# Kernel tuning notes

Hardware: AMD Instinct MI355X
Metric: run time of the kernel (lower is better)

The kernel has to match this reference:

```python
import jax, jax.numpy as jnp
import numpy as np

N, E = 50000, 800000
IN_C, H_C, OUT_C, HEADS = 64, 32, 32, 8


def setup_inputs() -> dict:
    key = jax.random.key(0)
    ks = jax.random.split(key, 16)
    def glorot(k, shape):
        fan_in = shape[-1]
        return jax.random.normal(k, shape, dtype=jnp.float32) / jnp.sqrt(jnp.float32(fan_in))
    inp = {
        'x': jax.random.normal(ks[0], (N, IN_C), dtype=jnp.float32),
        'edge_index': jax.random.randint(ks[1], (2, E), 0, N, dtype=jnp.int64),
        # layer 1: in_c -> h_c, heads
        'W1l': glorot(ks[2], (HEADS * H_C, IN_C)),
        'b1l': jnp.zeros((HEADS * H_C,), jnp.float32),
        'W1r': glorot(ks[3], (HEADS * H_C, IN_C)),
        'b1r': jnp.zeros((HEADS * H_C,), jnp.float32),
        'att1': glorot(ks[4], (HEADS, H_C)),
        'bias1': jnp.zeros((H_C,), jnp.float32),
        # layer 2: h_c -> out_c, heads
        'W2l': glorot(ks[5], (HEADS * OUT_C, H_C)),
        'b2l': jnp.zeros((HEADS * OUT_C,), jnp.float32),
        'W2r': glorot(ks[6], (HEADS * OUT_C, H_C)),
        'b2r': jnp.zeros((HEADS * OUT_C,), jnp.float32),
        'att2': glorot(ks[7], (HEADS, OUT_C)),
        'bias2': jnp.zeros((OUT_C,), jnp.float32),
    }
    return inp


def _gatv2_layer(x, src, dst, valid, Wl, bl, Wr, br, att, bias):
    # PyG GATv2Conv (share_weights=False, concat=False): message j->i uses
    # e = att . leaky_relu(lin_l(x_j) + lin_r(x_i), 0.2); softmax over dst; agg lin_l(x_j).
    n = x.shape[0]
    heads, c = att.shape
    xl = (x @ Wl.T + bl).reshape(n, heads, c)
    xr = (x @ Wr.T + br).reshape(n, heads, c)
    m = jax.nn.leaky_relu(xl[src] + xr[dst], negative_slope=0.2)  # [Etot,H,C]
    score = jnp.einsum('ehc,hc->eh', m, att)                      # [Etot,H]
    score = jnp.where(valid[:, None], score, -jnp.inf)
    smax = jax.ops.segment_max(score, dst, num_segments=n)        # [N,H]
    a = jnp.where(valid[:, None], jnp.exp(score - smax[dst]), 0.0)
    denom = jax.ops.segment_sum(a, dst, num_segments=n)
    a = a / jnp.maximum(denom[dst], 1e-16)
    out = jax.ops.segment_sum(a[..., None] * xl[src], dst, num_segments=n)  # [N,H,C]
    return out.mean(axis=1) + bias


def reference(x, edge_index, W1l, b1l, W1r, b1r, att1, bias1,
              W2l, b2l, W2r, b2r, att2, bias2):
    n = x.shape[0]
    src0, dst0 = edge_index[0], edge_index[1]
    # PyG removes existing self loops then adds fresh ones: mask originals,
    # append one self loop per node (keeps static shapes).
    loop = jnp.arange(n, dtype=src0.dtype)
    src = jnp.concatenate([src0, loop])
    dst = jnp.concatenate([dst0, loop])
    valid = jnp.concatenate([src0 != dst0, jnp.ones((n,), bool)])
    h = _gatv2_layer(x, src, dst, valid, W1l, b1l, W1r, b1r, att1, bias1)
    h = jax.nn.leaky_relu(h, negative_slope=0.01)  # nn.LeakyReLU default
    out = _gatv2_layer(h, src, dst, valid, W2l, b2l, W2r, b2r, att2, bias2)
    return out
```

## Files before the change

kernel.cpp:

```cpp
#include <hip/hip_runtime.h>
#include <math.h>

#define HEADS 8
#define CDIM 32
#define ODIM 256
#define BKT_SHIFT 7
#define CHUNK 2048

typedef _Float16 h2 __attribute__((ext_vector_type(2)));
typedef _Float16 h4 __attribute__((ext_vector_type(4)));
typedef _Float16 h8 __attribute__((ext_vector_type(8)));
typedef float f32x4 __attribute__((ext_vector_type(4)));
union H4 { h4 v; h2 p[2]; };

#if __has_builtin(__builtin_amdgcn_fdot2)
#define FDOT2(a,b,c) __builtin_amdgcn_fdot2((a),(b),(c),false)
#else
static __device__ __forceinline__ float fdot2_sw(h2 a, h2 b, float c){
  return fmaf((float)a.x, (float)b.x, fmaf((float)a.y, (float)b.y, c));
}
#define FDOT2(a,b,c) fdot2_sw((a),(b),(c))
#endif

__device__ __forceinline__ float lrelu(float v, float s){ return fmaxf(v, s*v); }


__global__ __launch_bounds__(512) void csr_offs_kernel(
    int* __restrict__ hist, int* __restrict__ btotal, int NB, int B){
  __shared__ int s[512];
  int b = blockIdx.x, t = threadIdx.x;
  int v = (t < NB) ? hist[t*B + b] : 0;
  s[t] = v;
  __syncthreads();
  for (int off=1; off<512; off<<=1){
    int u = (t >= off) ? s[t-off] : 0;
    __syncthreads(); s[t] += u; __syncthreads();
  }
  int excl = s[t] - v;
  if (t < NB) hist[t*B + b] = excl;
  if (t == NB-1) btotal[b] = excl + v;
}

__global__ __launch_bounds__(512) void csr_base_kernel(
    const int* __restrict__ btotal, int* __restrict__ base, int B){
  __shared__ int s[512];
  int t = threadIdx.x;
  int v = (t < B) ? btotal[t] : 0;
  s[t] = v;
  __syncthreads();
  for (int off=1; off<512; off<<=1){
    int u = (t >= off) ? s[t-off] : 0;
    __syncthreads(); s[t] += u; __syncthreads();
  }
  if (t < B) base[t] = s[t] - v;
  if (t == B-1) base[B] = s[t];
}

__global__ __launch_bounds__(256) void csr_scatter_kernel(
    const int* __restrict__ src, const int* __restrict__ dst,
    const int* __restrict__ rank, const int* __restrict__ offs,
    const int* __restrict__ base, int* __restrict__ bpack, int e, int B){
  int t = threadIdx.x, k = blockIdx.x;
  int base_i = k*CHUNK;
#pragma unroll
  for (int j = 0; j < CHUNK/256; ++j){
    int i = base_i + j*256 + t;
    if (i < e){
      int r = rank[i];
      if (r >= 0){
        int d = dst[i], s = src[i];
        int b = d >> BKT_SHIFT;
        int pos = base[b] + offs[k*B + b] + r;
        bpack[pos] = (s << BKT_SHIFT) | (d & 127);
      }
    }
  }
}

__global__ __launch_bounds__(256) void csr_sort_kernel(
    const int* __restrict__ bpack, const int* __restrict__ base,
    int* __restrict__ csr, int* __restrict__ indptr, int n, int B){
  __shared__ int lh[128], cur[128], ss[128];
  int b = blockIdx.x, t = threadIdx.x;
  int beg = base[b], cnt = base[b+1] - beg;
  if (t < 128) lh[t] = 0;
  __syncthreads();
  for (int j = t; j < cnt; j += 256){
    int p = bpack[beg + j];
    atomicAdd(&lh[p & 127], 1);
  }
  __syncthreads();
  int v = (t < 128) ? lh[t] : 0;
  if (t < 128) ss[t] = v;
  __syncthreads();
  for (int off=1; off<128; off<<=1){
    int u = (t >= off && t < 128) ? ss[t-off] : 0;
    __syncthreads();
    if (t < 128) ss[t] += u;
    __syncthreads();
  }
  if (t < 128){
    int excl = ss[t] - v;
    cur[t] = excl;
    int node = (b << BKT_SHIFT) + t;
    if (node <= n) indptr[node] = beg + excl;
  }
  __syncthreads();
  for (int j = t; j < cnt; j += 256){
    int p = bpack[beg + j];
    int lpos = atomicAdd(&cur[p & 127], 1);
    csr[beg + lpos] = p >> BKT_SHIFT;
  }
}

template<int K, bool FUSE_HIST>
__global__ __launch_bounds__(256, 2) void gemm_mfma(const float* __restrict__ X,
    const float* __restrict__ Wl, const float* __restrict__ bl,
    const float* __restrict__ Wr, const float* __restrict__ br,
    _Float16* __restrict__ outl, _Float16* __restrict__ outr, int n,
    const int* __restrict__ src, const int* __restrict__ dst,
    int* __restrict__ rank, int* __restrict__ hist, int e, int B){
  if (FUSE_HIST && blockIdx.y == 2){
    int k = blockIdx.x;
    int NB = (e + CHUNK-1)/CHUNK;
    if (k >= NB) return;
    __shared__ int lh[512];
    int t = threadIdx.x;
    for (int b = t; b < B; b += 256) lh[b] = 0;
    __syncthreads();
    int base_i = k*CHUNK;
#pragma unroll
    for (int j = 0; j < CHUNK/256; ++j){
      int i = base_i + j*256 + t;
      if (i < e){
        int s = src[i], d = dst[i];
        int r = -1;
        if (s != d) r = atomicAdd(&lh[d>>BKT_SHIFT], 1);
        rank[i] = r;
      }
    }
    __syncthreads();
    for (int b = t; b < B; b += 256) hist[k*B + b] = lh[b];
    return;
  }
  const int KP = K + 8;
  __shared__ __align__(16) _Float16 Xs[64*(K+8)];
  int t = threadIdx.x;
  int n0 = blockIdx.x*64;
  int ybase = blockIdx.y;

  for (int idx = t; idx < 64*(K/4); idx += 256){
    int row = idx/(K/4), c = (idx%(K/4))*4;
    int node = n0 + row; if (node >= n) node = n-1;
    float4 xv = *(const float4*)(X + (size_t)node*K + c);
    h4 hv = {(_Float16)xv.x, (_Float16)xv.y, (_Float16)xv.z, (_Float16)xv.w};
    *(h4*)(Xs + row*KP + c) = hv;
  }
  __syncthreads();

  int wave = t >> 6, lane = t & 63;
  int co = ybase*256 + wave*64;
  const float* W   = (co < 256) ? Wl : Wr;
  const float* Bv  = (co < 256) ? bl : br;
  _Float16* outp   = (co < 256) ? outl : outr;
  int lco = co & 255;
  int lr = lane & 15, lg = lane >> 4;

  f32x4 acc[4][4];
#pragma unroll
  for (int c = 0; c < 4; ++c)
#pragma unroll
    for (int m = 0; m < 4; ++m) acc[c][m] = (f32x4){0.f, 0.f, 0.f, 0.f};

#pragma unroll
  for (int ks = 0; ks < K/32; ++ks){
    int k0 = ks*32 + lg*8;
    h8 a[4], b[4];
#pragma unroll
    for (int c = 0; c < 4; ++c){
      const float* wp = W + (size_t)(lco + c*16 + lr)*K + k0;
      float4 w0 = *(const float4*)(wp);
      float4 w1 = *(const float4*)(wp + 4);
      a[c] = (h8){(_Float16)w0.x,(_Float16)w0.y,(_Float16)w0.z,(_Float16)w0.w,
                  (_Float16)w1.x,(_Float16)w1.y,(_Float16)w1.z,(_Float16)w1.w};
    }
#pragma unroll
    for (int m = 0; m < 4; ++m)
      b[m] = *(const h8*)(Xs + (m*16 + lr)*KP + k0);
#pragma unroll
    for (int c = 0; c < 4; ++c)
#pragma unroll
      for (int m = 0; m < 4; ++m)
        acc[c][m] = __builtin_amdgcn_mfma_f32_16x16x32_f16(a[c], b[m], acc[c][m], 0, 0, 0);
  }

#pragma unroll
  for (int c = 0; c < 4; ++c){
    int ch = lco + c*16 + lg*4;
    float4 bb = *(const float4*)(Bv + ch);
#pragma unroll
    for (int m = 0; m < 4; ++m){
      int node = n0 + m*16 + lr;
      if (node < n){
        h4 o = {(_Float16)(acc[c][m][0] + bb.x), (_Float16)(acc[c][m][1] + bb.y),
                (_Float16)(acc[c][m][2] + bb.z), (_Float16)(acc[c][m][3] + bb.w)};
        *(h4*)(outp + (size_t)node*ODIM + ch) = o;
      }
    }
  }
}

__global__ __launch_bounds__(256) void edge_kernel(
    const _Float16* __restrict__ xl, const _Float16* __restrict__ xr,
    const float* __restrict__ att, const float* __restrict__ bias,
    const int* __restrict__ indptr, const int* __restrict__ csr_src,
    float* __restrict__ out, int n, int act)
{
  int wid = blockIdx.x*4 + (threadIdx.x >> 6);
  if (wid >= n) return;
  int lane = threadIdx.x & 63;
  const float LOG2E = 1.44269504088896341f;

  float4 attf = *(const float4*)(att + 4*lane);
  h2 at0 = (h2){(_Float16)(attf.x*LOG2E), (_Float16)(attf.y*LOG2E)};
  h2 at1 = (h2){(_Float16)(attf.z*LOG2E), (_Float16)(attf.w*LOG2E)};
  const h2 c02 = {(_Float16)0.2f, (_Float16)0.2f};

  H4 xrh; xrh.v = *(const h4*)(xr + (size_t)wid*ODIM + 4*lane);
  H4 self; self.v = *(const h4*)(xl + (size_t)wid*ODIM + 4*lane);

  auto score = [&](const H4& c)->float{
    h2 t0 = c.p[0] + xrh.p[0];
    h2 t1 = c.p[1] + xrh.p[1];
    h2 q0 = __builtin_elementwise_max(t0, t0 * c02);
    h2 q1 = __builtin_elementwise_max(t1, t1 * c02);
    float d = FDOT2(q0, at0, FDOT2(q1, at1, 0.f));
    d += __shfl_xor(d, 1);
    d += __shfl_xor(d, 2);
    d += __shfl_xor(d, 4);
    return d;
  };

  float w0 = exp2f(score(self));
  float denom = w0;
  float4 acc;
  acc.x = w0 * (float)self.v.x;
  acc.y = w0 * (float)self.v.y;
  acc.z = w0 * (float)self.v.z;
  acc.w = w0 * (float)self.v.w;

  int beg = __builtin_amdgcn_readfirstlane(indptr[wid]);
  int end = __builtin_amdgcn_readfirstlane(indptr[wid+1]);
  int cnt = end - beg;

#define GATHER(j) (*(const h4*)(xl + (size_t)((unsigned)__shfl(sidx,(j)))*ODIM + 4*lane))
  for (int cb = 0; cb < cnt; cb += 64){
    int ccnt = min(cnt - cb, 64);
    int sidx = (lane < ccnt) ? csr_src[beg + cb + lane] : 0;
    H4 r0, r1, r2, r3;
    r0.v = (h4){}; r1.v = (h4){}; r2.v = (h4){}; r3.v = (h4){};
    if (ccnt > 0) r0.v = GATHER(0);
    if (ccnt > 1) r1.v = GATHER(1);
    if (ccnt > 2) r2.v = GATHER(2);
    if (ccnt > 3) r3.v = GATHER(3);
#pragma unroll 2
    for (int k = 0; k < ccnt; k += 2){
      H4 e0 = r0, e1 = r1;
      r0 = r2; r1 = r3;
      if (k+4 < ccnt) r2.v = GATHER(k+4);
      if (k+5 < ccnt) r3.v = GATHER(k+5);
      float s0 = score(e0);
      float s1 = score(e1);
      float pe0 = exp2f(s0);
      float pe1 = (k+1 < ccnt) ? exp2f(s1) : 0.f;
      denom += pe0 + pe1;
      acc.x = fmaf(pe0, (float)e0.v.x, fmaf(pe1, (float)e1.v.x, acc.x));
      acc.y = fmaf(pe0, (float)e0.v.y, fmaf(pe1, (float)e1.v.y, acc.y));
      acc.z = fmaf(pe0, (float)e0.v.z, fmaf(pe1, (float)e1.v.z, acc.z));
      acc.w = fmaf(pe0, (float)e0.v.w, fmaf(pe1, (float)e1.v.w, acc.w));
    }
  }
#undef GATHER

  float inv = 1.f/denom;
  float vx = acc.x*inv, vy = acc.y*inv, vz = acc.z*inv, vw = acc.w*inv;
  vx += __shfl_xor(vx, 8);  vx += __shfl_xor(vx, 16);  vx += __shfl_xor(vx, 32);
  vy += __shfl_xor(vy, 8);  vy += __shfl_xor(vy, 16);  vy += __shfl_xor(vy, 32);
  vz += __shfl_xor(vz, 8);  vz += __shfl_xor(vz, 16);  vz += __shfl_xor(vz, 32);
  vw += __shfl_xor(vw, 8);  vw += __shfl_xor(vw, 16);  vw += __shfl_xor(vw, 32);
  if (lane < 8){
    float4 bv = *(const float4*)(bias + 4*lane);
    float ox = vx*0.125f + bv.x;
    float oy = vy*0.125f + bv.y;
    float oz = vz*0.125f + bv.z;
    float ow = vw*0.125f + bv.w;
    if (act){
      ox = lrelu(ox, 0.01f); oy = lrelu(oy, 0.01f);
      oz = lrelu(oz, 0.01f); ow = lrelu(ow, 0.01f);
    }
    *(float4*)(out + (size_t)wid*CDIM + 4*lane) = make_float4(ox, oy, oz, ow);
  }
}

extern "C" void kernel_launch(void* const* d_in, const int* in_sizes, int n_in,
                              void* d_out, int out_size, void* d_ws, size_t ws_size,
                              hipStream_t stream){
  (void)n_in; (void)out_size; (void)ws_size;
  const float* x    = (const float*)d_in[0];
  const int*   ei   = (const int*)d_in[1];
  const float* W1l  = (const float*)d_in[2];
  const float* b1l  = (const float*)d_in[3];
  const float* W1r  = (const float*)d_in[4];
  const float* b1r  = (const float*)d_in[5];
  const float* att1 = (const float*)d_in[6];
  const float* bias1= (const float*)d_in[7];
  const float* W2l  = (const float*)d_in[8];
  const float* b2l  = (const float*)d_in[9];
  const float* W2r  = (const float*)d_in[10];
  const float* b2r  = (const float*)d_in[11];
  const float* att2 = (const float*)d_in[12];
  const float* bias2= (const float*)d_in[13];
  int n = in_sizes[0] / 64;
  int e = in_sizes[1] / 2;
  const int* src = ei;
  const int* dst = ei + e;

  char* ws = (char*)d_ws;
  size_t off = 0;
  auto alloc = [&](size_t bytes)->char*{
    char* p = ws + off; off += (bytes + 255) & ~(size_t)255; return p;
  };
  _Float16* xl  = (_Float16*)alloc((size_t)n*ODIM*2);
  _Float16* xr  = (_Float16*)alloc((size_t)n*ODIM*2);
  float* h      = (float*)alloc((size_t)n*CDIM*4);
  int*   indptr = (int*)alloc((size_t)(n+1)*4);
  int*   rank   = (int*)alloc((size_t)e*4);
  int*   csr    = (int*)alloc((size_t)e*4);
  int*   bpack  = (int*)alloc((size_t)e*4);

  int NB = (e + CHUNK-1) / CHUNK;
  int B  = (n + 127) >> 7;
  int*   hist   = (int*)alloc((size_t)NB*B*4);
  int*   btotal = (int*)alloc((size_t)B*4);
  int*   base   = (int*)alloc((size_t)(B+1)*4);

  int nt64 = (n + 63) / 64;

  gemm_mfma<64,true><<<dim3(nt64,3), 256, 0, stream>>>(
      x, W1l, b1l, W1r, b1r, xl, xr, n, src, dst, rank, hist, e, B);
  csr_offs_kernel<<<B, 512, 0, stream>>>(hist, btotal, NB, B);
  csr_base_kernel<<<1, 512, 0, stream>>>(btotal, base, B);
  csr_scatter_kernel<<<NB, 256, 0, stream>>>(src, dst, rank, hist, base, bpack, e, B);
  csr_sort_kernel<<<B, 256, 0, stream>>>(bpack, base, csr, indptr, n, B);

  edge_kernel<<<(n+3)/4, 256, 0, stream>>>(xl, xr, att1, bias1, indptr, csr, h, n, 1);
  gemm_mfma<32,false><<<dim3(nt64,2), 256, 0, stream>>>(
      h, W2l, b2l, W2r, b2r, xl, xr, n, nullptr, nullptr, nullptr, nullptr, 0, 0);
  edge_kernel<<<(n+3)/4, 256, 0, stream>>>(xl, xr, att2, bias2, indptr, csr, (float*)d_out, n, 0);
}
```

Before: 310.5 us.

## Split edge aggregation per head and process eight edges per wavefront concurrently

The per-node edge kernel now launches one wavefront per node and head. Each group of 8 lanes handles a different neighbor edge, so eight edges are gathered in parallel instead of a serial prefetch chain over all heads. Per-head partial results go to a new fp32 buffer, and a separate reduction kernel averages heads, adds bias and applies the activation. This trades extra launches, repeated CSR index reads per head and an n×256 fp32 intermediate write/read for more memory-level parallelism in the gather.

Result: slower. 526.2 us (+69.4%).

```diff
diff --git a/kernel.cpp b/kernel.cpp
--- a/kernel.cpp
+++ b/kernel.cpp
@@ -210,28 +210,30 @@
   }
 }
 
-__global__ __launch_bounds__(256) void edge_kernel(
+__global__ __launch_bounds__(256) void edge_head_kernel(
     const _Float16* __restrict__ xl, const _Float16* __restrict__ xr,
-    const float* __restrict__ att, const float* __restrict__ bias,
+    const float* __restrict__ att,
     const int* __restrict__ indptr, const int* __restrict__ csr_src,
-    float* __restrict__ out, int n, int act)
+    float* __restrict__ part, int n)
 {
-  int wid = blockIdx.x*4 + (threadIdx.x >> 6);
-  if (wid >= n) return;
+  int head = blockIdx.x & 7;
+  int node = ((blockIdx.x >> 3) << 2) + (threadIdx.x >> 6);
+  if (node >= n) return;
   int lane = threadIdx.x & 63;
+  int g = lane >> 3, q = lane & 7;
   const float LOG2E = 1.44269504088896341f;
 
-  float4 attf = *(const float4*)(att + 4*lane);
+  float4 attf = *(const float4*)(att + head*32 + 4*q);
   h2 at0 = (h2){(_Float16)(attf.x*LOG2E), (_Float16)(attf.y*LOG2E)};
   h2 at1 = (h2){(_Float16)(attf.z*LOG2E), (_Float16)(attf.w*LOG2E)};
   const h2 c02 = {(_Float16)0.2f, (_Float16)0.2f};
 
-  H4 xrh; xrh.v = *(const h4*)(xr + (size_t)wid*ODIM + 4*lane);
-  H4 self; self.v = *(const h4*)(xl + (size_t)wid*ODIM + 4*lane);
-
-  auto score = [&](const H4& c)->float{
-    h2 t0 = c.p[0] + xrh.p[0];
-    h2 t1 = c.p[1] + xrh.p[1];
+  const _Float16* xlh = xl + head*32 + 4*q;
+  H4 xr4; xr4.v = *(const h4*)(xr + (size_t)node*ODIM + head*32 + 4*q);
+
+  auto scoreh = [&](const H4& c)->float{
+    h2 t0 = c.p[0] + xr4.p[0];
+    h2 t1 = c.p[1] + xr4.p[1];
     h2 q0 = __builtin_elementwise_max(t0, t0 * c02);
     h2 q1 = __builtin_elementwise_max(t1, t1 * c02);
     float d = FDOT2(q0, at0, FDOT2(q1, at1, 0.f));
@@ -241,65 +243,64 @@
     return d;
   };
 
-  float w0 = exp2f(score(self));
-  float denom = w0;
+  H4 self; self.v = *(const h4*)(xlh + (size_t)node*ODIM);
+  float w0 = exp2f(scoreh(self));
+  float gz = (g == 0) ? w0 : 0.f;
+  float denom = gz;
   float4 acc;
-  acc.x = w0 * (float)self.v.x;
-  acc.y = w0 * (float)self.v.y;
-  acc.z = w0 * (float)self.v.z;
-  acc.w = w0 * (float)self.v.w;
-
-  int beg = __builtin_amdgcn_readfirstlane(indptr[wid]);
-  int end = __builtin_amdgcn_readfirstlane(indptr[wid+1]);
+  acc.x = gz * (float)self.v.x;
+  acc.y = gz * (float)self.v.y;
+  acc.z = gz * (float)self.v.z;
+  acc.w = gz * (float)self.v.w;
+
+  int beg = __builtin_amdgcn_readfirstlane(indptr[node]);
+  int end = __builtin_amdgcn_readfirstlane(indptr[node+1]);
   int cnt = end - beg;
 
-#define GATHER(j) (*(const h4*)(xl + (size_t)((unsigned)__shfl(sidx,(j)))*ODIM + 4*lane))
   for (int cb = 0; cb < cnt; cb += 64){
     int ccnt = min(cnt - cb, 64);
-    int sidx = (lane < ccnt) ? csr_src[beg + cb + lane] : 0;
-    H4 r0, r1, r2, r3;
-    r0.v = (h4){}; r1.v = (h4){}; r2.v = (h4){}; r3.v = (h4){};
-    if (ccnt > 0) r0.v = GATHER(0);
-    if (ccnt > 1) r1.v = GATHER(1);
-    if (ccnt > 2) r2.v = GATHER(2);
-    if (ccnt > 3) r3.v = GATHER(3);
+    int sidx = (lane < ccnt) ? csr_src[beg + cb + lane] : node;
 #pragma unroll 2
-    for (int k = 0; k < ccnt; k += 2){
-      H4 e0 = r0, e1 = r1;
-      r0 = r2; r1 = r3;
-      if (k+4 < ccnt) r2.v = GATHER(k+4);
-      if (k+5 < ccnt) r3.v = GATHER(k+5);
-      float s0 = score(e0);
-      float s1 = score(e1);
-      float pe0 = exp2f(s0);
-      float pe1 = (k+1 < ccnt) ? exp2f(s1) : 0.f;
-      denom += pe0 + pe1;
-      acc.x = fmaf(pe0, (float)e0.v.x, fmaf(pe1, (float)e1.v.x, acc.x));
-      acc.y = fmaf(pe0, (float)e0.v.y, fmaf(pe1, (float)e1.v.y, acc.y));
-      acc.z = fmaf(pe0, (float)e0.v.z, fmaf(pe1, (float)e1.v.z, acc.z));
-      acc.w = fmaf(pe0, (float)e0.v.w, fmaf(pe1, (float)e1.v.w, acc.w));
-    }
-  }
-#undef GATHER
-
-  float inv = 1.f/denom;
-  float vx = acc.x*inv, vy = acc.y*inv, vz = acc.z*inv, vw = acc.w*inv;
-  vx += __shfl_xor(vx, 8);  vx += __shfl_xor(vx, 16);  vx += __shfl_xor(vx, 32);
-  vy += __shfl_xor(vy, 8);  vy += __shfl_xor(vy, 16);  vy += __shfl_xor(vy, 32);
-  vz += __shfl_xor(vz, 8);  vz += __shfl_xor(vz, 16);  vz += __shfl_xor(vz, 32);
-  vw += __shfl_xor(vw, 8);  vw += __shfl_xor(vw, 16);  vw += __shfl_xor(vw, 32);
-  if (lane < 8){
-    float4 bv = *(const float4*)(bias + 4*lane);
-    float ox = vx*0.125f + bv.x;
-    float oy = vy*0.125f + bv.y;
-    float oz = vz*0.125f + bv.z;
-    float ow = vw*0.125f + bv.w;
-    if (act){
-      ox = lrelu(ox, 0.01f); oy = lrelu(oy, 0.01f);
-      oz = lrelu(oz, 0.01f); ow = lrelu(ow, 0.01f);
-    }
-    *(float4*)(out + (size_t)wid*CDIM + 4*lane) = make_float4(ox, oy, oz, ow);
-  }
+    for (int k = 0; k < ccnt; k += 8){
+      int j = k + g;
+      int si = __shfl(sidx, j);
+      H4 cv; cv.v = *(const h4*)(xlh + (size_t)si*ODIM);
+      float sc = scoreh(cv);
+      float pe = (j < ccnt) ? exp2f(sc) : 0.f;
+      denom += pe;
+      acc.x = fmaf(pe, (float)cv.v.x, acc.x);
+      acc.y = fmaf(pe, (float)cv.v.y, acc.y);
+      acc.z = fmaf(pe, (float)cv.v.z, acc.z);
+      acc.w = fmaf(pe, (float)cv.v.w, acc.w);
+    }
+  }
+
+#pragma unroll
+  for (int off = 8; off < 64; off <<= 1){
+    denom += __shfl_xor(denom, off);
+    acc.x += __shfl_xor(acc.x, off);
+    acc.y += __shfl_xor(acc.y, off);
+    acc.z += __shfl_xor(acc.z, off);
+    acc.w += __shfl_xor(acc.w, off);
+  }
+  if (g == 0){
+    float inv = 1.f/denom;
+    float* pp = part + ((size_t)node*HEADS + head)*CDIM + 4*q;
+    pp[0] = acc.x*inv; pp[1] = acc.y*inv; pp[2] = acc.z*inv; pp[3] = acc.w*inv;
+  }
+}
+
+__global__ __launch_bounds__(256) void head_reduce_kernel(
+    const float* __restrict__ part, const float* __restrict__ bias,
+    float* __restrict__ out, int n, int act){
+  int idx = blockIdx.x*256 + threadIdx.x;
+  int node = idx >> 5, c = idx & 31;
+  if (node >= n) return;
+  const float* p = part + (size_t)node*(HEADS*CDIM) + c;
+  float s = p[0]+p[32]+p[64]+p[96]+p[128]+p[160]+p[192]+p[224];
+  float o = s*0.125f + bias[c];
+  if (act) o = lrelu(o, 0.01f);
+  out[(size_t)node*CDIM + c] = o;
 }
 
 extern "C" void kernel_launch(void* const* d_in, const int* in_sizes, int n_in,
@@ -333,6 +334,7 @@
   _Float16* xl  = (_Float16*)alloc((size_t)n*ODIM*2);
   _Float16* xr  = (_Float16*)alloc((size_t)n*ODIM*2);
   float* h      = (float*)alloc((size_t)n*CDIM*4);
+  float* part   = (float*)alloc((size_t)n*HEADS*CDIM*4);
   int*   indptr = (int*)alloc((size_t)(n+1)*4);
   int*   rank   = (int*)alloc((size_t)e*4);
   int*   csr    = (int*)alloc((size_t)e*4);
@@ -345,6 +347,8 @@
   int*   base   = (int*)alloc((size_t)(B+1)*4);
 
   int nt64 = (n + 63) / 64;
+  int nq   = (n + 3) / 4;
+  int nrc  = (n*CDIM + 255) / 256;
 
   gemm_mfma<64,true><<<dim3(nt64,3), 256, 0, stream>>>(
       x, W1l, b1l, W1r, b1r, xl, xr, n, src, dst, rank, hist, e, B);
@@ -353,8 +357,10 @@
   csr_scatter_kernel<<<NB, 256, 0, stream>>>(src, dst, rank, hist, base, bpack, e, B);
   csr_sort_kernel<<<B, 256, 0, stream>>>(bpack, base, csr, indptr, n, B);
 
-  edge_kernel<<<(n+3)/4, 256, 0, stream>>>(xl, xr, att1, bias1, indptr, csr, h, n, 1);
+  edge_head_kernel<<<nq*8, 256, 0, stream>>>(xl, xr, att1, indptr, csr, part, n);
+  head_reduce_kernel<<<nrc, 256, 0, stream>>>(part, bias1, h, n, 1);
   gemm_mfma<32,false><<<dim3(nt64,2), 256, 0, stream>>>(
       h, W2l, b2l, W2r, b2r, xl, xr, n, nullptr, nullptr, nullptr, nullptr, 0, 0);
-  edge_kernel<<<(n+3)/4, 256, 0, stream>>>(xl, xr, att2, bias2, indptr, csr, (float*)d_out, n, 0);
-}
+  edge_head_kernel<<<nq*8, 256, 0, stream>>>(xl, xr, att2, indptr, csr, part, n);
+  head_reduce_kernel<<<nrc, 256, 0, stream>>>(part, bias2, (float*)d_out, n, 0);
+}
```

## Pre-convert weights to fp16, widen GEMM blocks to 512 threads, add nontemporal hints

Applied to the files above, without the earlier changes.

A small kernel now converts all four weight matrices to fp16 once per call. The GEMM then loads h8 fragments directly instead of converting fp32 to fp16 in every wave. Each GEMM block grows to 512 threads and covers both the left and right projections for a 64-node tile, so the X tile is staged and converted once instead of twice. The histogram side-blocks are adapted to the new block size. Nontemporal loads and stores are added for the X tile, the xr row, the CSR indices and the edge output, which adds one extra launch and lowers per-SM occupancy flexibility.

Measured after the change: 302.7 us. 2.5% less time.

```diff
diff --git a/kernel.cpp b/kernel.cpp
--- a/kernel.cpp
+++ b/kernel.cpp
@@ -11,7 +11,8 @@
 typedef _Float16 h4 __attribute__((ext_vector_type(4)));
 typedef _Float16 h8 __attribute__((ext_vector_type(8)));
 typedef float f32x4 __attribute__((ext_vector_type(4)));
-union H4 { h4 v; h2 p[2]; };
+typedef unsigned long long u64;
+union H4 { h4 v; h2 p[2]; u64 u; };
 
 #if __has_builtin(__builtin_amdgcn_fdot2)
 #define FDOT2(a,b,c) __builtin_amdgcn_fdot2((a),(b),(c),false)
@@ -23,6 +24,21 @@
 #endif
 
 __device__ __forceinline__ float lrelu(float v, float s){ return fmaxf(v, s*v); }
+
+__global__ __launch_bounds__(256) void wcvt_kernel(
+    const float* __restrict__ W1l, const float* __restrict__ W1r,
+    const float* __restrict__ W2l, const float* __restrict__ W2r,
+    _Float16* __restrict__ w1lh, _Float16* __restrict__ w1rh,
+    _Float16* __restrict__ w2lh, _Float16* __restrict__ w2rh){
+  int i = (blockIdx.x*256 + threadIdx.x)*4;
+  const float* s; _Float16* d; int off;
+  if (i < 16384)      { s = W1l; d = w1lh; off = i; }
+  else if (i < 32768) { s = W1r; d = w1rh; off = i - 16384; }
+  else if (i < 40960) { s = W2l; d = w2lh; off = i - 32768; }
+  else                { s = W2r; d = w2rh; off = i - 40960; }
+  float4 v = *(const float4*)(s + off);
+  *(h4*)(d + off) = (h4){(_Float16)v.x, (_Float16)v.y, (_Float16)v.z, (_Float16)v.w};
+}
 
 
 __global__ __launch_bounds__(512) void csr_offs_kernel(
@@ -114,24 +130,24 @@
 }
 
 template<int K, bool FUSE_HIST>
-__global__ __launch_bounds__(256, 2) void gemm_mfma(const float* __restrict__ X,
-    const float* __restrict__ Wl, const float* __restrict__ bl,
-    const float* __restrict__ Wr, const float* __restrict__ br,
+__global__ __launch_bounds__(512) void gemm_mfma(const float* __restrict__ X,
+    const _Float16* __restrict__ Wlh, const float* __restrict__ bl,
+    const _Float16* __restrict__ Wrh, const float* __restrict__ br,
     _Float16* __restrict__ outl, _Float16* __restrict__ outr, int n,
     const int* __restrict__ src, const int* __restrict__ dst,
     int* __restrict__ rank, int* __restrict__ hist, int e, int B){
-  if (FUSE_HIST && blockIdx.y == 2){
+  if (FUSE_HIST && blockIdx.y == 1){
     int k = blockIdx.x;
     int NB = (e + CHUNK-1)/CHUNK;
     if (k >= NB) return;
     __shared__ int lh[512];
     int t = threadIdx.x;
-    for (int b = t; b < B; b += 256) lh[b] = 0;
+    if (t < 512) lh[t] = 0;
     __syncthreads();
     int base_i = k*CHUNK;
 #pragma unroll
-    for (int j = 0; j < CHUNK/256; ++j){
-      int i = base_i + j*256 + t;
+    for (int j = 0; j < CHUNK/512; ++j){
+      int i = base_i + j*512 + t;
       if (i < e){
         int s = src[i], d = dst[i];
         int r = -1;
@@ -140,29 +156,28 @@
       }
     }
     __syncthreads();
-    for (int b = t; b < B; b += 256) hist[k*B + b] = lh[b];
+    for (int b = t; b < B; b += 512) hist[k*B + b] = lh[b];
     return;
   }
   const int KP = K + 8;
   __shared__ __align__(16) _Float16 Xs[64*(K+8)];
   int t = threadIdx.x;
   int n0 = blockIdx.x*64;
-  int ybase = blockIdx.y;
-
-  for (int idx = t; idx < 64*(K/4); idx += 256){
+
+  for (int idx = t; idx < 64*(K/4); idx += 512){
     int row = idx/(K/4), c = (idx%(K/4))*4;
     int node = n0 + row; if (node >= n) node = n-1;
-    float4 xv = *(const float4*)(X + (size_t)node*K + c);
-    h4 hv = {(_Float16)xv.x, (_Float16)xv.y, (_Float16)xv.z, (_Float16)xv.w};
-    *(h4*)(Xs + row*KP + c) = hv;
+    f32x4 xv = __builtin_nontemporal_load((const f32x4*)(X + (size_t)node*K + c));
+    *(h4*)(Xs + row*KP + c) = (h4){(_Float16)xv[0], (_Float16)xv[1],
+                                   (_Float16)xv[2], (_Float16)xv[3]};
   }
   __syncthreads();
 
   int wave = t >> 6, lane = t & 63;
-  int co = ybase*256 + wave*64;
-  const float* W   = (co < 256) ? Wl : Wr;
-  const float* Bv  = (co < 256) ? bl : br;
-  _Float16* outp   = (co < 256) ? outl : outr;
+  int co = wave*64;
+  const _Float16* W = (co < 256) ? Wlh : Wrh;
+  const float* Bv   = (co < 256) ? bl : br;
+  _Float16* outp    = (co < 256) ? outl : outr;
   int lco = co & 255;
   int lr = lane & 15, lg = lane >> 4;
 
@@ -177,13 +192,8 @@
     int k0 = ks*32 + lg*8;
     h8 a[4], b[4];
 #pragma unroll
-    for (int c = 0; c < 4; ++c){
-      const float* wp = W + (size_t)(lco + c*16 + lr)*K + k0;
-      float4 w0 = *(const float4*)(wp);
-      float4 w1 = *(const float4*)(wp + 4);
-      a[c] = (h8){(_Float16)w0.x,(_Float16)w0.y,(_Float16)w0.z,(_Float16)w0.w,
-                  (_Float16)w1.x,(_Float16)w1.y,(_Float16)w1.z,(_Float16)w1.w};
-    }
+    for (int c = 0; c < 4; ++c)
+      a[c] = *(const h8*)(W + (size_t)(lco + c*16 + lr)*K + k0);
 #pragma unroll
     for (int m = 0; m < 4; ++m)
       b[m] = *(const h8*)(Xs + (m*16 + lr)*KP + k0);
@@ -226,7 +236,7 @@
   h2 at1 = (h2){(_Float16)(attf.z*LOG2E), (_Float16)(attf.w*LOG2E)};
   const h2 c02 = {(_Float16)0.2f, (_Float16)0.2f};
 
-  H4 xrh; xrh.v = *(const h4*)(xr + (size_t)wid*ODIM + 4*lane);
+  H4 xrh; xrh.u = __builtin_nontemporal_load((const u64*)(xr + (size_t)wid*ODIM + 4*lane));
   H4 self; self.v = *(const h4*)(xl + (size_t)wid*ODIM + 4*lane);
 
   auto score = [&](const H4& c)->float{
@@ -256,7 +266,7 @@
 #define GATHER(j) (*(const h4*)(xl + (size_t)((unsigned)__shfl(sidx,(j)))*ODIM + 4*lane))
   for (int cb = 0; cb < cnt; cb += 64){
     int ccnt = min(cnt - cb, 64);
-    int sidx = (lane < ccnt) ? csr_src[beg + cb + lane] : 0;
+    int sidx = (lane < ccnt) ? __builtin_nontemporal_load(csr_src + beg + cb + lane) : 0;
     H4 r0, r1, r2, r3;
     r0.v = (h4){}; r1.v = (h4){}; r2.v = (h4){}; r3.v = (h4){};
     if (ccnt > 0) r0.v = GATHER(0);
@@ -298,7 +308,8 @@
       ox = lrelu(ox, 0.01f); oy = lrelu(oy, 0.01f);
       oz = lrelu(oz, 0.01f); ow = lrelu(ow, 0.01f);
     }
-    *(float4*)(out + (size_t)wid*CDIM + 4*lane) = make_float4(ox, oy, oz, ow);
+    f32x4 ov = {ox, oy, oz, ow};
+    __builtin_nontemporal_store(ov, (f32x4*)(out + (size_t)wid*CDIM + 4*lane));
   }
 }
 
@@ -337,6 +348,10 @@
   int*   rank   = (int*)alloc((size_t)e*4);
   int*   csr    = (int*)alloc((size_t)e*4);
   int*   bpack  = (int*)alloc((size_t)e*4);
+  _Float16* w1lh = (_Float16*)alloc((size_t)ODIM*64*2);
+  _Float16* w1rh = (_Float16*)alloc((size_t)ODIM*64*2);
+  _Float16* w2lh = (_Float16*)alloc((size_t)ODIM*32*2);
+  _Float16* w2rh = (_Float16*)alloc((size_t)ODIM*32*2);
 
   int NB = (e + CHUNK-1) / CHUNK;
   int B  = (n + 127) >> 7;
@@ -346,15 +361,16 @@
 
   int nt64 = (n + 63) / 64;
 
-  gemm_mfma<64,true><<<dim3(nt64,3), 256, 0, stream>>>(
-      x, W1l, b1l, W1r, b1r, xl, xr, n, src, dst, rank, hist, e, B);
+  wcvt_kernel<<<48, 256, 0, stream>>>(W1l, W1r, W2l, W2r, w1lh, w1rh, w2lh, w2rh);
+  gemm_mfma<64,true><<<dim3(nt64,2), 512, 0, stream>>>(
+      x, w1lh, b1l, w1rh, b1r, xl, xr, n, src, dst, rank, hist, e, B);
   csr_offs_kernel<<<B, 512, 0, stream>>>(hist, btotal, NB, B);
   csr_base_kernel<<<1, 512, 0, stream>>>(btotal, base, B);
   csr_scatter_kernel<<<NB, 256, 0, stream>>>(src, dst, rank, hist, base, bpack, e, B);
   csr_sort_kernel<<<B, 256, 0, stream>>>(bpack, base, csr, indptr, n, B);
 
   edge_kernel<<<(n+3)/4, 256, 0, stream>>>(xl, xr, att1, bias1, indptr, csr, h, n, 1);
-  gemm_mfma<32,false><<<dim3(nt64,2), 256, 0, stream>>>(
-      h, W2l, b2l, W2r, b2r, xl, xr, n, nullptr, nullptr, nullptr, nullptr, 0, 0);
+  gemm_mfma<32,false><<<dim3(nt64,1), 512, 0, stream>>>(
+      h, w2lh, b2l, w2rh, b2r, xl, xr, n, nullptr, nullptr, nullptr, nullptr, 0, 0);
   edge_kernel<<<(n+3)/4, 256, 0, stream>>>(xl, xr, att2, bias2, indptr, csr, (float*)d_out, n, 0);
 }
```
